# Kernel optimization log

Measured on AMD Instinct MI355X. Metric: run time of the kernel, lower is better.

The kernel has to match this reference:

```python
import jax, jax.numpy as jnp
import numpy as np

D_MODEL = 768
H = 12
D_K = D_MODEL // H
B = 2
S = 2048
NEG = -1e9


def setup_inputs() -> dict:
    key = jax.random.key(0)
    ks = jax.random.split(key, 12)
    scale = 1.0 / np.sqrt(D_MODEL)
    inp = {
        "q": jax.random.normal(ks[0], (B, S, D_MODEL), jnp.float32),
        "k": jax.random.normal(ks[1], (B, S, D_MODEL), jnp.float32),
        "v": jax.random.normal(ks[2], (B, S, D_MODEL), jnp.float32),
        "mask": jax.random.randint(ks[3], (B, 1, S, S), 0, 2, jnp.int32),
        "Wq": jax.random.normal(ks[4], (D_MODEL, D_MODEL), jnp.float32) * scale,
        "bq": jnp.zeros((D_MODEL,), jnp.float32),
        "Wk": jax.random.normal(ks[5], (D_MODEL, D_MODEL), jnp.float32) * scale,
        "bk": jnp.zeros((D_MODEL,), jnp.float32),
        "Wv": jax.random.normal(ks[6], (D_MODEL, D_MODEL), jnp.float32) * scale,
        "bv": jnp.zeros((D_MODEL,), jnp.float32),
        "Wo": jax.random.normal(ks[7], (D_MODEL, D_MODEL), jnp.float32) * scale,
        "bo": jnp.zeros((D_MODEL,), jnp.float32),
    }
    return inp


def _split_heads(x):
    # [B, S, D] -> [B, H, S, D_K]
    b, s, _ = x.shape
    return x.reshape(b, s, H, D_K).transpose(0, 2, 1, 3)


def reference(q, k, v, mask, Wq, bq, Wk, bk, Wv, bv, Wo, bo):
    # torch Linear: x @ W.T + b
    query = _split_heads(q @ Wq.T + bq)
    key_ = _split_heads(k @ Wk.T + bk)
    value = _split_heads(v @ Wv.T + bv)

    scores = jnp.einsum("bhqd,bhkd->bhqk", query, key_) / np.sqrt(D_K)
    scores = jnp.where(mask == 0, NEG, scores)
    attn = jax.nn.softmax(scores, axis=-1)  # dropout p=0.0 -> identity

    x = jnp.einsum("bhqk,bhkd->bhqd", attn, value)
    x = x.transpose(0, 2, 1, 3).reshape(q.shape[0], -1, D_MODEL)
    return x @ Wo.T + bo
```

## Files before the change

### kernel.cpp

```cpp
#include <hip/hip_runtime.h>
#include <math.h>

#define DMODEL 768
#define NHEAD 12
#define DKDIM 64
#define BB 2
#define SS 2048
#define MROWS (BB * SS)
#define WELEM (DMODEL * DMODEL)
#define KCHUNK (SS / 2)
#define MWORDS (SS / 64)

typedef unsigned short bf16_t;
typedef __attribute__((ext_vector_type(8))) short s8;
typedef __attribute__((ext_vector_type(4))) float f4;

#define MFMA(a, b, c) __builtin_amdgcn_mfma_f32_16x16x32_bf16((a), (b), (c), 0, 0, 0)

__device__ __forceinline__ bf16_t f2bf(float f) {
    unsigned u = __float_as_uint(f);
    u += 0x7fffu + ((u >> 16) & 1u);
    return (bf16_t)(u >> 16);
}
__device__ __forceinline__ unsigned pack2(float a, float b) {
    return (unsigned)f2bf(a) | ((unsigned)f2bf(b) << 16);
}
__device__ __forceinline__ s8 ldfrag(const bf16_t* p) {
    union { uint4 u; s8 s; } x;
    x.u = *(const uint4*)p;
    return x.s;
}

__device__ __forceinline__ void ld_stage(const bf16_t* p, uint4& u0, uint4& u1) {
    u0 = *(const uint4*)p;
    u1 = *(const uint4*)(p + 8);
}
__device__ __forceinline__ void ld_stage(const float* p, uint4& u0, uint4& u1) {
    const float4 f0 = *(const float4*)p;
    const float4 f1 = *(const float4*)(p + 4);
    const float4 f2 = *(const float4*)(p + 8);
    const float4 f3 = *(const float4*)(p + 12);
    u0.x = pack2(f0.x, f0.y); u0.y = pack2(f0.z, f0.w);
    u0.z = pack2(f1.x, f1.y); u0.w = pack2(f1.z, f1.w);
    u1.x = pack2(f2.x, f2.y); u1.y = pack2(f2.z, f2.w);
    u1.z = pack2(f3.x, f3.y); u1.w = pack2(f3.z, f3.w);
}

__global__ void cvt_weights(const float* __restrict__ W0, const float* __restrict__ W1,
                            const float* __restrict__ W2, const float* __restrict__ W3,
                            bf16_t* __restrict__ dst)
{
    const float* src = (blockIdx.y == 0) ? W0 : (blockIdx.y == 1) ? W1
                     : (blockIdx.y == 2) ? W2 : W3;
    bf16_t* d = dst + (size_t)blockIdx.y * WELEM;
    const int i = (blockIdx.x * 256 + threadIdx.x) * 4;
    const float4 v = *(const float4*)(src + i);
    ushort4 h;
    h.x = f2bf(v.x); h.y = f2bf(v.y); h.z = f2bf(v.z); h.w = f2bf(v.w);
    *(ushort4*)(d + i) = h;
}

__global__ __launch_bounds__(256) void mask_to_bits(
    const int* __restrict__ mask, unsigned long long* __restrict__ mbits)
{
    const size_t gid = (size_t)blockIdx.x * 256 + threadIdx.x;
    const int m = mask[gid];
    const unsigned long long bal = __ballot(m != 0);
    if ((threadIdx.x & 63) == 0) mbits[gid >> 6] = bal;
}

template<typename TA, typename TO>
__global__ __launch_bounds__(256) void gemm_tiled(
    const TA* __restrict__ A0, const TA* __restrict__ A1, const TA* __restrict__ A2,
    const bf16_t* __restrict__ W0, const bf16_t* __restrict__ W1, const bf16_t* __restrict__ W2,
    const float* __restrict__ bias0, const float* __restrict__ bias1, const float* __restrict__ bias2,
    TO* __restrict__ C0, TO* __restrict__ C1, TO* __restrict__ C2,
    float sc0, float sc1, float sc2)
{
    __shared__ uint4 As4[128 * 4];
    __shared__ uint4 Bs4[128 * 4];

    const int z = blockIdx.z;
    const TA*     A    = (z == 0) ? A0 : (z == 1) ? A1 : A2;
    const bf16_t* W    = (z == 0) ? W0 : (z == 1) ? W1 : W2;
    const float*  bias = (z == 0) ? bias0 : (z == 1) ? bias1 : bias2;
    TO*           C    = (z == 0) ? C0 : (z == 1) ? C1 : C2;
    const float   sc   = (z == 0) ? sc0 : (z == 1) ? sc1 : sc2;

    const int tid  = threadIdx.x;
    const int lane = tid & 63;
    const int w    = tid >> 6;
    const int wm   = w & 1;
    const int wn   = w >> 1;
    const int l15  = lane & 15;
    const int quad = lane >> 4;
    const int m0   = blockIdx.y * 128;
    const int n0   = blockIdx.x * 128;

    const int srow  = tid >> 1;
    const int shalf = tid & 1;
    const int sw    = srow & 3;

    const TA*     aptr = A + (size_t)(m0 + srow) * DMODEL + shalf * 16;
    const bf16_t* wptr = W + (size_t)(n0 + srow) * DMODEL + shalf * 16;

    f4 acc[4][4];
    #pragma unroll
    for (int i = 0; i < 4; i++)
        #pragma unroll
        for (int j = 0; j < 4; j++)
            acc[i][j] = (f4){0.f, 0.f, 0.f, 0.f};

    for (int k0 = 0; k0 < DMODEL; k0 += 32) {
        uint4 au0, au1, bu0, bu1;
        ld_stage(aptr + k0, au0, au1);
        ld_stage(wptr + k0, bu0, bu1);
        __syncthreads();
        As4[srow * 4 + ((shalf * 2 + 0) ^ sw)] = au0;
        As4[srow * 4 + ((shalf * 2 + 1) ^ sw)] = au1;
        Bs4[srow * 4 + ((shalf * 2 + 0) ^ sw)] = bu0;
        Bs4[srow * 4 + ((shalf * 2 + 1) ^ sw)] = bu1;
        __syncthreads();

        s8 af[4], bf[4];
        #pragma unroll
        for (int t = 0; t < 4; t++) {
            const int ar = wm * 64 + t * 16 + l15;
            const int br = wn * 64 + t * 16 + l15;
            union { uint4 u; s8 s; } xa, xb;
            xa.u = As4[ar * 4 + (quad ^ (ar & 3))];
            xb.u = Bs4[br * 4 + (quad ^ (br & 3))];
            af[t] = xa.s;
            bf[t] = xb.s;
        }
        #pragma unroll
        for (int mt = 0; mt < 4; mt++)
            #pragma unroll
            for (int nt = 0; nt < 4; nt++)
                acc[mt][nt] = MFMA(af[mt], bf[nt], acc[mt][nt]);
    }

    #pragma unroll
    for (int mt = 0; mt < 4; mt++) {
        #pragma unroll
        for (int nt = 0; nt < 4; nt++) {
            const int col = n0 + wn * 64 + nt * 16 + l15;
            const float bb = bias[col];
            #pragma unroll
            for (int reg = 0; reg < 4; reg++) {
                const int row = m0 + wm * 64 + mt * 16 + quad * 4 + reg;
                const float val = (acc[mt][nt][reg] + bb) * sc;
                TO* dst = C + (size_t)row * DMODEL + col;
                if constexpr (sizeof(TO) == 2) *dst = f2bf(val);
                else                           *dst = val;
            }
        }
    }
}

__global__ __launch_bounds__(512) void attn_mfma(
    const bf16_t* __restrict__ Q, const bf16_t* __restrict__ K,
    const bf16_t* __restrict__ V, const unsigned long long* __restrict__ mbits,
    bf16_t* __restrict__ O)
{
    __shared__ unsigned Vs[2][64][36];
    __shared__ unsigned Ps[8][16][36];
    __shared__ float    Msh[8][16], Lsh[8][16];

    const int tid  = threadIdx.x;
    const int lane = tid & 63;
    const int w    = tid >> 6;
    const int wq   = w & 3;
    const int ws   = w >> 2;
    const int l15  = lane & 15;
    const int quad = lane >> 4;
    const int q0   = blockIdx.x * 64;
    const int h    = blockIdx.y;
    const int b    = blockIdx.z;
    const int ks   = ws * KCHUNK;
    const size_t base = ((size_t)b * SS) * DMODEL + (size_t)h * DKDIM;

    const bf16_t* qrow = Q + base + (size_t)(q0 + wq * 16 + l15) * DMODEL + quad * 8;
    const s8 qf0 = ldfrag(qrow);
    const s8 qf1 = ldfrag(qrow + 32);

    f4 oacc[4];
    float m_run[4], l_run[4];
    #pragma unroll
    for (int i = 0; i < 4; i++) {
        oacc[i] = (f4){0.f, 0.f, 0.f, 0.f};
        m_run[i] = -3.0e30f; l_run[i] = 0.0f;
    }

    const int kp  = tid & 31;
    const int oct = (tid >> 5) & 7;
    const bf16_t* vbase = V + base + (size_t)(2 * kp) * DMODEL + oct * 8;

    const unsigned long long* mbase =
        mbits + ((size_t)b * SS + (q0 + wq * 16 + quad * 4)) * MWORDS;

    uint4 va = *(const uint4*)(vbase + (size_t)ks * DMODEL);
    uint4 vb = *(const uint4*)(vbase + (size_t)ks * DMODEL + DMODEL);

    for (int k0 = ks; k0 < ks + KCHUNK; k0 += 64) {
        __syncthreads();
        {
            const unsigned short* pa = (const unsigned short*)&va;
            const unsigned short* pb = (const unsigned short*)&vb;
            #pragma unroll
            for (int i = 0; i < 8; i++)
                Vs[ws][oct * 8 + i][kp] = (unsigned)pa[i] | ((unsigned)pb[i] << 16);
        }
        if (k0 + 64 < ks + KCHUNK) {
            va = *(const uint4*)(vbase + (size_t)(k0 + 64) * DMODEL);
            vb = *(const uint4*)(vbase + (size_t)(k0 + 64) * DMODEL + DMODEL);
        }
        unsigned long long mw[4];
        #pragma unroll
        for (int reg = 0; reg < 4; reg++)
            mw[reg] = mbase[(size_t)reg * MWORDS + (k0 >> 6)];

        f4 sacc[4];
        #pragma unroll
        for (int nt = 0; nt < 4; nt++) {
            const bf16_t* krow = K + base + (size_t)(k0 + nt * 16 + l15) * DMODEL + quad * 8;
            f4 zz2 = {0.f, 0.f, 0.f, 0.f};
            zz2 = MFMA(qf0, ldfrag(krow), zz2);
            zz2 = MFMA(qf1, ldfrag(krow + 32), zz2);
            sacc[nt] = zz2;
        }

        #pragma unroll
        for (int reg = 0; reg < 4; reg++) {
            const unsigned mlo = ((unsigned)mw[reg]) >> l15;
            const unsigned mhi = ((unsigned)(mw[reg] >> 32)) >> l15;
            float sv[4];
            sv[0] = (mlo & 1u)       ? sacc[0][reg] : -1.0e9f;
            sv[1] = (mlo & 0x10000u) ? sacc[1][reg] : -1.0e9f;
            sv[2] = (mhi & 1u)       ? sacc[2][reg] : -1.0e9f;
            sv[3] = (mhi & 0x10000u) ? sacc[3][reg] : -1.0e9f;

            float mx = fmaxf(fmaxf(sv[0], sv[1]), fmaxf(sv[2], sv[3]));
            mx = fmaxf(mx, __shfl_xor(mx, 1, 16));
            mx = fmaxf(mx, __shfl_xor(mx, 2, 16));
            mx = fmaxf(mx, __shfl_xor(mx, 4, 16));
            mx = fmaxf(mx, __shfl_xor(mx, 8, 16));

            const float m_new = fmaxf(m_run[reg], mx);
            const float alpha = __expf(m_run[reg] - m_new);
            float p[4];
            float rs = 0.f;
            #pragma unroll
            for (int nt = 0; nt < 4; nt++) {
                p[nt] = __expf(sv[nt] - m_new);
                rs += p[nt];
            }
            rs += __shfl_xor(rs, 1, 16);
            rs += __shfl_xor(rs, 2, 16);
            rs += __shfl_xor(rs, 4, 16);
            rs += __shfl_xor(rs, 8, 16);

            l_run[reg] = l_run[reg] * alpha + rs;
            m_run[reg] = m_new;
            #pragma unroll
            for (int dt = 0; dt < 4; dt++) oacc[dt][reg] *= alpha;

            #pragma unroll
            for (int nt = 0; nt < 4; nt++) {
                const float mine  = p[nt];
                const float other = __shfl_xor(mine, 1, 16);
                if ((lane & 1) == 0)
                    Ps[w][quad * 4 + reg][nt * 8 + (l15 >> 1)] = pack2(mine, other);
            }
        }
        __syncthreads();

        #pragma unroll
        for (int kt = 0; kt < 2; kt++) {
            union { uint4 u; s8 s; } pf;
            pf.u = *(const uint4*)&Ps[w][l15][kt * 16 + quad * 4];
            #pragma unroll
            for (int dt = 0; dt < 4; dt++) {
                union { uint4 u; s8 s; } vf;
                vf.u = *(const uint4*)&Vs[ws][dt * 16 + l15][kt * 16 + quad * 4];
                oacc[dt] = MFMA(pf.s, vf.s, oacc[dt]);
            }
        }
    }

    if (l15 == 0) {
        #pragma unroll
        for (int reg = 0; reg < 4; reg++) {
            Msh[w][quad * 4 + reg] = m_run[reg];
            Lsh[w][quad * 4 + reg] = l_run[reg];
        }
    }
    __syncthreads();

    float scale[4];
    #pragma unroll
    for (int reg = 0; reg < 4; reg++) {
        const float m_o = Msh[w ^ 4][quad * 4 + reg];
        const float l_o = Lsh[w ^ 4][quad * 4 + reg];
        const float m_t = fmaxf(m_run[reg], m_o);
        const float w_s = __expf(m_run[reg] - m_t);
        const float w_o = __expf(m_o - m_t);
        const float l_t = l_run[reg] * w_s + l_o * w_o;
        scale[reg] = w_s / l_t;
    }
    #pragma unroll
    for (int dt = 0; dt < 4; dt++)
        #pragma unroll
        for (int reg = 0; reg < 4; reg++)
            oacc[dt][reg] *= scale[reg];

    float (*Osh)[16][66] = (float (*)[16][66])Ps;
    if (ws == 1) {
        #pragma unroll
        for (int dt = 0; dt < 4; dt++)
            #pragma unroll
            for (int reg = 0; reg < 4; reg++)
                Osh[wq][quad * 4 + reg][dt * 16 + l15] = oacc[dt][reg];
    }
    __syncthreads();

    if (ws == 0) {
        #pragma unroll
        for (int reg = 0; reg < 4; reg++) {
            const size_t row = q0 + wq * 16 + quad * 4 + reg;
            #pragma unroll
            for (int dt = 0; dt < 4; dt++) {
                const float val = oacc[dt][reg] + Osh[wq][quad * 4 + reg][dt * 16 + l15];
                O[base + row * DMODEL + dt * 16 + l15] = f2bf(val);
            }
        }
    }
}

extern "C" void kernel_launch(void* const* d_in, const int* in_sizes, int n_in,
                              void* d_out, int out_size, void* d_ws, size_t ws_size,
                              hipStream_t stream)
{
    const float* q    = (const float*)d_in[0];
    const float* k    = (const float*)d_in[1];
    const float* v    = (const float*)d_in[2];
    const int*   mask = (const int*)  d_in[3];
    const float* Wq   = (const float*)d_in[4];
    const float* bq   = (const float*)d_in[5];
    const float* Wk   = (const float*)d_in[6];
    const float* bk   = (const float*)d_in[7];
    const float* Wv   = (const float*)d_in[8];
    const float* bv   = (const float*)d_in[9];
    const float* Wo   = (const float*)d_in[10];
    const float* bo   = (const float*)d_in[11];
    float* out = (float*)d_out;

    bf16_t* wsb = (bf16_t*)d_ws;
    const size_t plane = (size_t)MROWS * DMODEL;
    bf16_t* Qp  = wsb;
    bf16_t* Kp  = wsb + plane;
    bf16_t* Vp  = wsb + 2 * plane;
    bf16_t* Ctx = wsb + 3 * plane;
    bf16_t* Wqb = wsb + 4 * plane;
    bf16_t* Wkb = Wqb + WELEM;
    bf16_t* Wvb = Wkb + WELEM;
    bf16_t* Wob = Wvb + WELEM;
    unsigned long long* mbits = (unsigned long long*)(Wob + WELEM);

    cvt_weights<<<dim3(WELEM / 1024, 4), 256, 0, stream>>>(Wq, Wk, Wv, Wo, Wqb);
    mask_to_bits<<<dim3((BB * SS * SS) / 256), 256, 0, stream>>>(mask, mbits);

    gemm_tiled<float, bf16_t><<<dim3(DMODEL / 128, MROWS / 128, 3), 256, 0, stream>>>(
        q, k, v, Wqb, Wkb, Wvb, bq, bk, bv, Qp, Kp, Vp, 0.125f, 1.0f, 1.0f);

    attn_mfma<<<dim3(SS / 64, NHEAD, BB), 512, 0, stream>>>(Qp, Kp, Vp, mbits, Ctx);

    gemm_tiled<bf16_t, float><<<dim3(DMODEL / 128, MROWS / 128, 1), 256, 0, stream>>>(
        Ctx, Ctx, Ctx, Wob, Wob, Wob, bo, bo, bo, out, out, out, 1.0f, 1.0f, 1.0f);
}
```

Baseline: 374.4 us.

## Write V projection transposed per head and load V fragments directly from global

The QKV projection GEMM now writes the V output in a per-head transposed layout [B,H,DK,S], so the attention kernel can load V MFMA fragments straight from global memory. This removes the shared-memory V staging, its register prefetch, and two block-wide barriers per key tile. In exchange, V fragments are read from global/L2 on every tile without an explicit prefetch, and the GEMM epilogue for V does strided 4-byte stores across rows of length S.

```diff
diff --git a/kernel.cpp b/kernel.cpp
--- a/kernel.cpp
+++ b/kernel.cpp
@@ -75,7 +75,7 @@
     const bf16_t* __restrict__ W0, const bf16_t* __restrict__ W1, const bf16_t* __restrict__ W2,
     const float* __restrict__ bias0, const float* __restrict__ bias1, const float* __restrict__ bias2,
     TO* __restrict__ C0, TO* __restrict__ C1, TO* __restrict__ C2,
-    float sc0, float sc1, float sc2)
+    float sc0, float sc1, float sc2, int vtz)
 {
     __shared__ uint4 As4[128 * 4];
     __shared__ uint4 Bs4[128 * 4];
@@ -142,17 +142,35 @@
 
     #pragma unroll
     for (int mt = 0; mt < 4; mt++) {
+        const int grow = m0 + wm * 64 + mt * 16 + quad * 4;
         #pragma unroll
         for (int nt = 0; nt < 4; nt++) {
             const int col = n0 + wn * 64 + nt * 16 + l15;
             const float bb = bias[col];
-            #pragma unroll
-            for (int reg = 0; reg < 4; reg++) {
-                const int row = m0 + wm * 64 + mt * 16 + quad * 4 + reg;
-                const float val = (acc[mt][nt][reg] + bb) * sc;
-                TO* dst = C + (size_t)row * DMODEL + col;
-                if constexpr (sizeof(TO) == 2) *dst = f2bf(val);
-                else                           *dst = val;
+            bool done = false;
+            if constexpr (sizeof(TO) == 2) {
+                if (z == vtz) {
+                    const int bidx = grow >> 11;
+                    const int s0   = grow & (SS - 1);
+                    const float v0 = acc[mt][nt][0] + bb;
+                    const float v1 = acc[mt][nt][1] + bb;
+                    const float v2 = acc[mt][nt][2] + bb;
+                    const float v3 = acc[mt][nt][3] + bb;
+                    unsigned* dst = (unsigned*)((bf16_t*)C +
+                        ((size_t)(bidx * NHEAD + (col >> 6)) * DKDIM + (col & 63)) * SS + s0);
+                    dst[0] = pack2(v0, v1);
+                    dst[1] = pack2(v2, v3);
+                    done = true;
+                }
+            }
+            if (!done) {
+                #pragma unroll
+                for (int reg = 0; reg < 4; reg++) {
+                    const float val = (acc[mt][nt][reg] + bb) * sc;
+                    TO* dst = C + (size_t)(grow + reg) * DMODEL + col;
+                    if constexpr (sizeof(TO) == 2) *dst = f2bf(val);
+                    else                           *dst = val;
+                }
             }
         }
     }
@@ -160,10 +178,9 @@
 
 __global__ __launch_bounds__(512) void attn_mfma(
     const bf16_t* __restrict__ Q, const bf16_t* __restrict__ K,
-    const bf16_t* __restrict__ V, const unsigned long long* __restrict__ mbits,
+    const bf16_t* __restrict__ Vt, const unsigned long long* __restrict__ mbits,
     bf16_t* __restrict__ O)
 {
-    __shared__ unsigned Vs[2][64][36];
     __shared__ unsigned Ps[8][16][36];
     __shared__ float    Msh[8][16], Lsh[8][16];
 
@@ -179,6 +196,7 @@
     const int b    = blockIdx.z;
     const int ks   = ws * KCHUNK;
     const size_t base = ((size_t)b * SS) * DMODEL + (size_t)h * DKDIM;
+    const bf16_t* vtb = Vt + (size_t)(b * NHEAD + h) * DKDIM * SS;
 
     const bf16_t* qrow = Q + base + (size_t)(q0 + wq * 16 + l15) * DMODEL + quad * 8;
     const s8 qf0 = ldfrag(qrow);
@@ -192,29 +210,10 @@
         m_run[i] = -3.0e30f; l_run[i] = 0.0f;
     }
 
-    const int kp  = tid & 31;
-    const int oct = (tid >> 5) & 7;
-    const bf16_t* vbase = V + base + (size_t)(2 * kp) * DMODEL + oct * 8;
-
     const unsigned long long* mbase =
         mbits + ((size_t)b * SS + (q0 + wq * 16 + quad * 4)) * MWORDS;
 
-    uint4 va = *(const uint4*)(vbase + (size_t)ks * DMODEL);
-    uint4 vb = *(const uint4*)(vbase + (size_t)ks * DMODEL + DMODEL);
-
     for (int k0 = ks; k0 < ks + KCHUNK; k0 += 64) {
-        __syncthreads();
-        {
-            const unsigned short* pa = (const unsigned short*)&va;
-            const unsigned short* pb = (const unsigned short*)&vb;
-            #pragma unroll
-            for (int i = 0; i < 8; i++)
-                Vs[ws][oct * 8 + i][kp] = (unsigned)pa[i] | ((unsigned)pb[i] << 16);
-        }
-        if (k0 + 64 < ks + KCHUNK) {
-            va = *(const uint4*)(vbase + (size_t)(k0 + 64) * DMODEL);
-            vb = *(const uint4*)(vbase + (size_t)(k0 + 64) * DMODEL + DMODEL);
-        }
         unsigned long long mw[4];
         #pragma unroll
         for (int reg = 0; reg < 4; reg++)
@@ -273,7 +272,6 @@
                     Ps[w][quad * 4 + reg][nt * 8 + (l15 >> 1)] = pack2(mine, other);
             }
         }
-        __syncthreads();
 
         #pragma unroll
         for (int kt = 0; kt < 2; kt++) {
@@ -281,9 +279,9 @@
             pf.u = *(const uint4*)&Ps[w][l15][kt * 16 + quad * 4];
             #pragma unroll
             for (int dt = 0; dt < 4; dt++) {
-                union { uint4 u; s8 s; } vf;
-                vf.u = *(const uint4*)&Vs[ws][dt * 16 + l15][kt * 16 + quad * 4];
-                oacc[dt] = MFMA(pf.s, vf.s, oacc[dt]);
+                const s8 vf = ldfrag(vtb + (size_t)(dt * 16 + l15) * SS
+                                         + k0 + kt * 32 + quad * 8);
+                oacc[dt] = MFMA(pf.s, vf, oacc[dt]);
             }
         }
     }
@@ -359,7 +357,7 @@
     const size_t plane = (size_t)MROWS * DMODEL;
     bf16_t* Qp  = wsb;
     bf16_t* Kp  = wsb + plane;
-    bf16_t* Vp  = wsb + 2 * plane;
+    bf16_t* Vtp = wsb + 2 * plane;
     bf16_t* Ctx = wsb + 3 * plane;
     bf16_t* Wqb = wsb + 4 * plane;
     bf16_t* Wkb = Wqb + WELEM;
@@ -371,10 +369,10 @@
     mask_to_bits<<<dim3((BB * SS * SS) / 256), 256, 0, stream>>>(mask, mbits);
 
     gemm_tiled<float, bf16_t><<<dim3(DMODEL / 128, MROWS / 128, 3), 256, 0, stream>>>(
-        q, k, v, Wqb, Wkb, Wvb, bq, bk, bv, Qp, Kp, Vp, 0.125f, 1.0f, 1.0f);
-
-    attn_mfma<<<dim3(SS / 64, NHEAD, BB), 512, 0, stream>>>(Qp, Kp, Vp, mbits, Ctx);
+        q, k, v, Wqb, Wkb, Wvb, bq, bk, bv, Qp, Kp, Vtp, 0.125f, 1.0f, 1.0f, 2);
+
+    attn_mfma<<<dim3(SS / 64, NHEAD, BB), 512, 0, stream>>>(Qp, Kp, Vtp, mbits, Ctx);
 
     gemm_tiled<bf16_t, float><<<dim3(DMODEL / 128, MROWS / 128, 1), 256, 0, stream>>>(
-        Ctx, Ctx, Ctx, Wob, Wob, Wob, bo, bo, bo, out, out, out, 1.0f, 1.0f, 1.0f);
-}
+        Ctx, Ctx, Ctx, Wob, Wob, Wob, bo, bo, bo, out, out, out, 1.0f, 1.0f, 1.0f, -1);
+}
```

After: 415.9 us. 11.1% more time.
